# Kernel optimization log

Hardware: AMD Instinct MI355X
Metric: run time of the kernel (lower is better)

The kernel has to match this reference:

```python
import jax, jax.numpy as jnp
import numpy as np

N_NODES = 100000
F_IN = 128
HID = 64
N_EDGES = 1600000
N_PAIRS = 500000


def setup_inputs() -> dict:
    key = jax.random.key(0)
    ks = jax.random.split(key, 12)
    x = jax.random.normal(ks[0], (N_NODES, F_IN), dtype=jnp.float32)
    edge_index = jax.random.randint(ks[1], (2, N_EDGES), 0, N_NODES, dtype=jnp.int32)
    edge_pairs = jax.random.randint(ks[2], (2, N_PAIRS), 0, N_NODES, dtype=jnp.int32)
    # GCNConv weights (glorot-ish scale) and biases
    W1 = jax.random.normal(ks[3], (F_IN, HID), dtype=jnp.float32) / np.sqrt(F_IN)
    b1 = jnp.zeros((HID,), dtype=jnp.float32)
    W2 = jax.random.normal(ks[4], (HID, HID), dtype=jnp.float32) / np.sqrt(HID)
    b2 = jnp.zeros((HID,), dtype=jnp.float32)
    # link predictor MLP: Linear(2H -> H), ReLU, Linear(H -> 1), Sigmoid
    lpW1 = jax.random.normal(ks[5], (2 * HID, HID), dtype=jnp.float32) / np.sqrt(2 * HID)
    lpb1 = jnp.zeros((HID,), dtype=jnp.float32)
    lpW2 = jax.random.normal(ks[6], (HID, 1), dtype=jnp.float32) / np.sqrt(HID)
    lpb2 = jnp.zeros((1,), dtype=jnp.float32)
    return {"x": x, "edge_index": edge_index, "edge_pairs": edge_pairs,
            "W1": W1, "b1": b1, "W2": W2, "b2": b2,
            "lpW1": lpW1, "lpb1": lpb1, "lpW2": lpW2, "lpb2": lpb2}


def _gcn_layer(h, W, b, row, col, deg_inv_sqrt, n_nodes):
    # PyG GCNConv: h' = D^{-1/2} (A + I) D^{-1/2} (h W) + b
    h = h @ W                                   # [N, out]
    norm = deg_inv_sqrt[row] * deg_inv_sqrt[col]  # [E']
    msg = h[row] * norm[:, None]                # gather + scale, [E', out]
    out = jax.ops.segment_sum(msg, col, num_segments=n_nodes)
    return out + b


def reference(x, edge_index, edge_pairs, W1, b1, W2, b2, lpW1, lpb1, lpW2, lpb2):
    n = x.shape[0]
    # add self-loops once (shared by both layers since graph is fixed)
    loop = jnp.arange(n, dtype=edge_index.dtype)
    row = jnp.concatenate([edge_index[0], loop])
    col = jnp.concatenate([edge_index[1], loop])
    deg = jnp.zeros((n,), dtype=x.dtype).at[col].add(1.0)
    deg_inv_sqrt = jnp.where(deg > 0, jax.lax.rsqrt(jnp.maximum(deg, 1.0)), 0.0)

    h = _gcn_layer(x, W1, b1, row, col, deg_inv_sqrt, n)
    h = jax.nn.relu(h)            # dropout is identity at inference
    h = _gcn_layer(h, W2, b2, row, col, deg_inv_sqrt, n)

    # link scorer: gather node pairs, concat, MLP, sigmoid
    z = jnp.concatenate([h[edge_pairs[0]], h[edge_pairs[1]]], axis=1)  # [P, 2H]
    z = jax.nn.relu(z @ lpW1 + lpb1)
    logits = z @ lpW2 + lpb2      # [P, 1]
    return jax.nn.sigmoid(logits).squeeze(-1)
```

## Files before the change

### kernel.cpp

```cpp
#include <hip/hip_runtime.h>
#include <cstddef>
#include <cstdint>

typedef float f4 __attribute__((ext_vector_type(4)));
typedef unsigned short us4 __attribute__((ext_vector_type(4)));
typedef short s8v __attribute__((ext_vector_type(8)));

#define HID 64
#define EPB 4096
#define CAP2 16384

__device__ inline float b2f(unsigned short u) {
    union { unsigned u32; float f; } x; x.u32 = (unsigned)u << 16; return x.f;
}
__device__ inline unsigned short f2b(float f) {
    union { float f; unsigned u; } x; x.f = f;
    unsigned r = 0x7FFFu + ((x.u >> 16) & 1u);
    return (unsigned short)((x.u + r) >> 16);
}
__device__ inline f4 b2f4(us4 h) { f4 r; r[0]=b2f(h[0]); r[1]=b2f(h[1]); r[2]=b2f(h[2]); r[3]=b2f(h[3]); return r; }
__device__ inline us4 f2b4(f4 v) { us4 r; r[0]=f2b(v[0]); r[1]=f2b(v[1]); r[2]=f2b(v[2]); r[3]=f2b(v[3]); return r; }

__device__ inline f4 ld4(const float* p) { return *(const f4*)p; }
__device__ inline f4 ld4(const unsigned short* p) { return b2f4(*(const us4*)p); }
__device__ inline void st4(float* p, f4 v) { *(f4*)p = v; }
__device__ inline void st4(unsigned short* p, f4 v) { *(us4*)p = f2b4(v); }

__global__ __launch_bounds__(256) void k_initcur(int* gcur) {
    int i = blockIdx.x * 256 + threadIdx.x;
    if (i < 512) gcur[i] = i * CAP2;
}

__global__ __launch_bounds__(512) void k_partB(const int* __restrict__ row,
                                               const int* __restrict__ col,
                                               int* __restrict__ gcur,
                                               unsigned* __restrict__ buf, int E) {
    __shared__ int h[512];
    __shared__ int lo[512];
    __shared__ int lb[512];
    __shared__ int lcur[512];
    __shared__ unsigned lbuf[EPB];
    __shared__ unsigned short bk[EPB];
    int t = threadIdx.x;
    h[t] = 0;
    __syncthreads();
    int e0 = blockIdx.x * EPB, e1 = min(E, e0 + EPB);
    for (int i = e0 + t * 4; i < e1; i += 2048) {
        int4 c = *(const int4*)(col + i);
        atomicAdd(&h[c.x >> 9], 1);
        atomicAdd(&h[c.y >> 9], 1);
        atomicAdd(&h[c.z >> 9], 1);
        atomicAdd(&h[c.w >> 9], 1);
    }
    __syncthreads();
    int v = h[t];
    lo[t] = v;
    __syncthreads();
    for (int o = 1; o < 512; o <<= 1) {
        int x = (t >= o) ? lo[t - o] : 0;
        __syncthreads();
        lo[t] += x;
        __syncthreads();
    }
    int excl = lo[t] - v;
    lb[t] = v ? atomicAdd(&gcur[t], v) : 0;
    __syncthreads();
    lo[t] = excl;
    lcur[t] = excl;
    __syncthreads();
    for (int i = e0 + t * 4; i < e1; i += 2048) {
        int4 c = *(const int4*)(col + i);
        int4 r = *(const int4*)(row + i);
        int b0 = c.x >> 9; int p0 = atomicAdd(&lcur[b0], 1);
        lbuf[p0] = ((unsigned)(c.x & 511) << 17) | (unsigned)r.x; bk[p0] = (unsigned short)b0;
        int b1 = c.y >> 9; int p1 = atomicAdd(&lcur[b1], 1);
        lbuf[p1] = ((unsigned)(c.y & 511) << 17) | (unsigned)r.y; bk[p1] = (unsigned short)b1;
        int b2 = c.z >> 9; int p2 = atomicAdd(&lcur[b2], 1);
        lbuf[p2] = ((unsigned)(c.z & 511) << 17) | (unsigned)r.z; bk[p2] = (unsigned short)b2;
        int b3 = c.w >> 9; int p3 = atomicAdd(&lcur[b3], 1);
        lbuf[p3] = ((unsigned)(c.w & 511) << 17) | (unsigned)r.w; bk[p3] = (unsigned short)b3;
    }
    __syncthreads();
    int n = e1 - e0;
    for (int i = t; i < n; i += 512) {
        int b = bk[i];
        buf[lb[b] + (i - lo[b])] = lbuf[i];
    }
}

__global__ __launch_bounds__(512) void k_scanB(const int* __restrict__ gcur,
                                               int* __restrict__ gbase, int NB, int E) {
    __shared__ int s[512];
    int t = threadIdx.x;
    int v = (t < NB) ? (gcur[t] - t * CAP2) : 0;
    s[t] = v;
    __syncthreads();
    for (int o = 1; o < 512; o <<= 1) {
        int x = (t >= o) ? s[t - o] : 0;
        __syncthreads();
        s[t] += x;
        __syncthreads();
    }
    if (t < NB) gbase[t] = s[t] - v;
    if (t == 0) gbase[NB] = E;
}

__global__ __launch_bounds__(512) void k_passC(const unsigned* __restrict__ buf,
                                               const int* __restrict__ gcur,
                                               const int* __restrict__ gbase,
                                               int* __restrict__ rowptr,
                                               int* __restrict__ srcs,
                                               float* __restrict__ dis, int N, int E) {
    __shared__ unsigned sbuf[CAP2];
    __shared__ int hist[512];
    __shared__ int off[512];
    __shared__ int cur[512];
    int b = blockIdx.x, t = threadIdx.x;
    int r0 = b * CAP2, r1 = gcur[b];
    int n = r1 - r0;
    int w0 = gbase[b];
    hist[t] = 0;
    __syncthreads();
    for (int i = r0 + t; i < r1; i += 512) atomicAdd(&hist[(buf[i] >> 17) & 511], 1);
    __syncthreads();
    int v = hist[t];
    off[t] = v;
    __syncthreads();
    for (int o = 1; o < 512; o <<= 1) {
        int x = (t >= o) ? off[t - o] : 0;
        __syncthreads();
        off[t] += x;
        __syncthreads();
    }
    int excl = off[t] - v;
    int gc = b * 512 + t;
    if (gc < N) {
        rowptr[gc] = w0 + excl;
        dis[gc] = rsqrtf(1.0f + (float)v);
    }
    if (b == (int)gridDim.x - 1 && t == 0) rowptr[N] = E;
    cur[t] = excl;
    __syncthreads();
    for (int i = r0 + t; i < r1; i += 512) {
        unsigned u = buf[i];
        int pos = atomicAdd(&cur[(u >> 17) & 511], 1);
        sbuf[pos] = u & 0x1FFFF;
    }
    __syncthreads();
    for (int i = t; i < n; i += 512) srcs[w0 + i] = (int)sbuf[i];
}

template<int K, int NC, typename TIN>
__global__ __launch_bounds__(256) void k_gemmM(
    const TIN* __restrict__ X, const float* __restrict__ W,
    const float* __restrict__ bias, const float* __restrict__ scale,
    unsigned short* __restrict__ outA, unsigned short* __restrict__ outB, int N)
{
    constexpr int KP = K + 8;
    __shared__ unsigned short xs[64][KP];
    __shared__ unsigned short wt[NC][KP];
    const int t = threadIdx.x;
    const int lane = t & 63;
    const int wv = t >> 6;
    const int nbase = blockIdx.x * 64;

    if constexpr (sizeof(TIN) == 4) {
        for (int idx = t; idx < 64 * K / 4; idx += 256) {
            int row = idx / (K / 4);
            int kc = (idx % (K / 4)) * 4;
            int g = nbase + row;
            f4 v = {0.f, 0.f, 0.f, 0.f};
            if (g < N) v = *(const f4*)((const float*)X + (size_t)g * K + kc);
            *(us4*)&xs[row][kc] = f2b4(v);
        }
    } else {
        for (int idx = t; idx < 64 * K / 8; idx += 256) {
            int row = idx / (K / 8);
            int kc = (idx % (K / 8)) * 8;
            int g = nbase + row;
            uint4 v = {0u, 0u, 0u, 0u};
            if (g < N) v = *(const uint4*)((const unsigned short*)X + (size_t)g * K + kc);
            *(uint4*)&xs[row][kc] = v;
        }
    }
    constexpr int WROWS = K * NC / 64;
    for (int idx = t; idx < WROWS * 16; idx += 256) {
        int ks = idx >> 4;
        int c4 = (idx & 15) * 4;
        f4 v = *(const f4*)(W + (size_t)ks * 64 + c4);
        int cofs = (NC == 128 && ks >= K) ? 64 : 0;
        int kk = ks & (K - 1);
        #pragma unroll
        for (int j = 0; j < 4; ++j)
            wt[c4 + j + cofs][kk] = f2b(v[j]);
    }
    __syncthreads();

    constexpr int NT = NC / 16;
    f4 acc[NT];
    #pragma unroll
    for (int i = 0; i < NT; ++i) acc[i] = (f4){0.f, 0.f, 0.f, 0.f};

    const int l15 = lane & 15;
    const int kbase = (lane >> 4) * 8;
    #pragma unroll
    for (int kt = 0; kt < K / 32; ++kt) {
        s8v a = *(const s8v*)&xs[wv * 16 + l15][kt * 32 + kbase];
        #pragma unroll
        for (int ct = 0; ct < NT; ++ct) {
            s8v b = *(const s8v*)&wt[ct * 16 + l15][kt * 32 + kbase];
            acc[ct] = __builtin_amdgcn_mfma_f32_16x16x32_bf16(a, b, acc[ct], 0, 0, 0);
        }
    }

    const int r0 = (lane >> 4) * 4;
    #pragma unroll
    for (int r = 0; r < 4; ++r) {
        int g = nbase + wv * 16 + r0 + r;
        if (g >= N) continue;
        float sc = scale ? scale[g] : 1.0f;
        #pragma unroll
        for (int ct = 0; ct < NT; ++ct) {
            int c = ct * 16 + l15;
            float v = acc[ct][r] * sc;
            if (c < 64) {
                if (bias) v += bias[c];
                outA[(size_t)g * 64 + c] = f2b(v);
            } else {
                outB[(size_t)g * 64 + (c - 64)] = f2b(v);
            }
        }
    }
}

__global__ __launch_bounds__(256) void k_gather(
    const unsigned short* __restrict__ g, const int* __restrict__ rowptr,
    const int* __restrict__ srcs, const float* __restrict__ dis,
    const float* __restrict__ bias, unsigned short* __restrict__ out, int N, int do_relu)
{
    int t = blockIdx.x * 256 + threadIdx.x;
    int node = t >> 4;
    if (node >= N) return;
    int c4 = (t & 15) * 4;

    f4 a0 = ld4(g + (size_t)node * HID + c4);
    f4 a1 = {0.f, 0.f, 0.f, 0.f};
    f4 a2 = {0.f, 0.f, 0.f, 0.f};
    f4 a3 = {0.f, 0.f, 0.f, 0.f};
    int s = rowptr[node], e = rowptr[node + 1];
    for (; s + 3 < e; s += 4) {
        int r0 = srcs[s], r1 = srcs[s + 1], r2 = srcs[s + 2], r3 = srcs[s + 3];
        a0 += ld4(g + (size_t)r0 * HID + c4);
        a1 += ld4(g + (size_t)r1 * HID + c4);
        a2 += ld4(g + (size_t)r2 * HID + c4);
        a3 += ld4(g + (size_t)r3 * HID + c4);
    }
    for (; s < e; ++s) a0 += ld4(g + (size_t)srcs[s] * HID + c4);
    a0 = (a0 + a1) + (a2 + a3);

    float sc = dis[node];
    f4 r;
    #pragma unroll
    for (int j = 0; j < 4; ++j) {
        r[j] = a0[j] * sc + bias[c4 + j];
        if (do_relu) r[j] = r[j] > 0.f ? r[j] : 0.f;
    }
    st4(out + (size_t)node * HID + c4, r);
}

template<int K, typename TIN, typename TOUT>
__global__ __launch_bounds__(256) void k_gemm(
    const TIN* __restrict__ X, const float* __restrict__ W,
    const float* __restrict__ bias, const float* __restrict__ scale,
    TOUT* __restrict__ out1, TOUT* __restrict__ out2, int N)
{
    __shared__ float xs[64][68];
    __shared__ float ws[64][64];
    const int t = threadIdx.x;
    const int nbase = blockIdx.x * 64;
    const int c4 = (t & 15) * 4;
    const int n4 = (t >> 4) * 4;

    float acc[4][4] = {{0.f,0.f,0.f,0.f},{0.f,0.f,0.f,0.f},{0.f,0.f,0.f,0.f},{0.f,0.f,0.f,0.f}};

    const int node = t & 63;
    const int gn = nbase + node;
    const TIN* Xrow = (gn < N) ? (X + (size_t)gn * K) : nullptr;
    const f4* W4 = (const f4*)W;

    for (int kt = 0; kt < K / 64; ++kt) {
        __syncthreads();
        #pragma unroll
        for (int i = 0; i < 4; ++i) {
            int k4r = i * 4 + (t >> 6);
            f4 v = {0.f, 0.f, 0.f, 0.f};
            if (Xrow) v = ld4(Xrow + (size_t)(kt * 16 + k4r) * 4);
            xs[k4r * 4 + 0][node] = v[0];
            xs[k4r * 4 + 1][node] = v[1];
            xs[k4r * 4 + 2][node] = v[2];
            xs[k4r * 4 + 3][node] = v[3];
        }
        #pragma unroll
        for (int i = 0; i < 4; ++i) {
            int f = i * 256 + t;
            int k = f >> 4, m4 = f & 15;
            *(f4*)&ws[k][m4 * 4] = W4[(size_t)(kt * 64 + k) * 16 + m4];
        }
        __syncthreads();
        #pragma unroll 8
        for (int k = 0; k < 64; ++k) {
            f4 xv = *(const f4*)&xs[k][n4];
            f4 wv = *(const f4*)&ws[k][c4];
            #pragma unroll
            for (int i2 = 0; i2 < 4; ++i2)
                #pragma unroll
                for (int j = 0; j < 4; ++j)
                    acc[i2][j] += xv[i2] * wv[j];
        }
    }

    #pragma unroll
    for (int i = 0; i < 4; ++i) {
        int g = nbase + n4 + i;
        if (g < N) {
            float s = scale ? scale[g] : 1.0f;
            f4 r;
            #pragma unroll
            for (int j = 0; j < 4; ++j) {
                float b = bias ? bias[c4 + j] : 0.0f;
                r[j] = acc[i][j] * s + b;
            }
            st4(out1 + (size_t)g * HID + c4, r);
            if (out2) st4(out2 + (size_t)g * HID + c4, r);
        }
    }
}

template<typename TIN>
__global__ __launch_bounds__(256) void k_gemm2(
    const TIN* __restrict__ X, const float* __restrict__ W,
    const float* __restrict__ bias,
    unsigned short* __restrict__ outA, unsigned short* __restrict__ outB, int N)
{
    __shared__ float xs[64][68];
    __shared__ float ws[64][128];
    const int t = threadIdx.x;
    const int nbase = blockIdx.x * 64;
    const int c4 = (t & 15) * 4;
    const int n4 = (t >> 4) * 4;

    float accA[4][4] = {{0.f,0.f,0.f,0.f},{0.f,0.f,0.f,0.f},{0.f,0.f,0.f,0.f},{0.f,0.f,0.f,0.f}};
    float accB[4][4] = {{0.f,0.f,0.f,0.f},{0.f,0.f,0.f,0.f},{0.f,0.f,0.f,0.f},{0.f,0.f,0.f,0.f}};

    const int node = t & 63;
    const int gn = nbase + node;
    const TIN* Xrow = (gn < N) ? (X + (size_t)gn * HID) : nullptr;
    const f4* W4 = (const f4*)W;

    #pragma unroll
    for (int i = 0; i < 4; ++i) {
        int k4r = i * 4 + (t >> 6);
        f4 v = {0.f, 0.f, 0.f, 0.f};
        if (Xrow) v = ld4(Xrow + (size_t)k4r * 4);
        xs[k4r * 4 + 0][node] = v[0];
        xs[k4r * 4 + 1][node] = v[1];
        xs[k4r * 4 + 2][node] = v[2];
        xs[k4r * 4 + 3][node] = v[3];
    }
    #pragma unroll
    for (int i = 0; i < 8; ++i) {
        int f = i * 256 + t;
        int r = f >> 4, m4 = f & 15;
        int k = r & 63, half = (r >> 6) * 64;
        *(f4*)&ws[k][half + m4 * 4] = W4[f];
    }
    __syncthreads();
    #pragma unroll 8
    for (int k = 0; k < 64; ++k) {
        f4 xv = *(const f4*)&xs[k][n4];
        f4 wa = *(const f4*)&ws[k][c4];
        f4 wb = *(const f4*)&ws[k][64 + c4];
        #pragma unroll
        for (int i2 = 0; i2 < 4; ++i2)
            #pragma unroll
            for (int j = 0; j < 4; ++j) {
                accA[i2][j] += xv[i2] * wa[j];
                accB[i2][j] += xv[i2] * wb[j];
            }
    }

    #pragma unroll
    for (int i = 0; i < 4; ++i) {
        int g = nbase + n4 + i;
        if (g < N) {
            f4 ra, rb;
            #pragma unroll
            for (int j = 0; j < 4; ++j) {
                ra[j] = accA[i][j] + bias[c4 + j];
                rb[j] = accB[i][j];
            }
            st4(outA + (size_t)g * HID + c4, ra);
            st4(outB + (size_t)g * HID + c4, rb);
        }
    }
}

__global__ __launch_bounds__(256) void k_count(const int* __restrict__ col,
                                               float* __restrict__ deg, int E) {
    int e = blockIdx.x * 256 + threadIdx.x;
    if (e < E) unsafeAtomicAdd(&deg[col[e]], 1.0f);
}
__global__ __launch_bounds__(256) void k_initf(float* p, float v, int n) {
    int i = blockIdx.x * 256 + threadIdx.x;
    if (i < n) p[i] = v;
}
__global__ __launch_bounds__(256) void k_rsqrt(float* deg, int N) {
    int i = blockIdx.x * 256 + threadIdx.x;
    if (i < N) deg[i] = rsqrtf(deg[i]);
}
__global__ __launch_bounds__(256) void k_scatter(
    const float* __restrict__ g, const int* __restrict__ row, const int* __restrict__ col,
    float* __restrict__ acc, int E)
{
    int t = blockIdx.x * 256 + threadIdx.x;
    int e = t >> 4;
    if (e >= E) return;
    int c4 = (t & 15) * 4;
    int r = row[e], c = col[e];
    f4 v = *(const f4*)(g + (size_t)r * HID + c4);
    float* dst = acc + (size_t)c * HID + c4;
    unsafeAtomicAdd(dst + 0, v[0]);
    unsafeAtomicAdd(dst + 1, v[1]);
    unsafeAtomicAdd(dst + 2, v[2]);
    unsafeAtomicAdd(dst + 3, v[3]);
}
__global__ __launch_bounds__(256) void k_finish(
    const float* __restrict__ acc, const float* __restrict__ dis, const float* __restrict__ bias,
    float* __restrict__ out, int N, int do_relu)
{
    int t = blockIdx.x * 256 + threadIdx.x;
    if (t >= N * 16) return;
    int node = t >> 4, c4 = (t & 15) * 4;
    float s = dis[node];
    f4 v = *(const f4*)(acc + (size_t)t * 4);
    f4 r;
    #pragma unroll
    for (int j = 0; j < 4; ++j) {
        r[j] = v[j] * s + bias[c4 + j];
        if (do_relu) r[j] = r[j] > 0.f ? r[j] : 0.f;
    }
    *(f4*)(out + (size_t)t * 4) = r;
}

__global__ __launch_bounds__(256) void k_pair(
    const unsigned short* __restrict__ A, const unsigned short* __restrict__ B,
    const int* __restrict__ pairs, const float* __restrict__ w2, const float* __restrict__ b2,
    float* __restrict__ out, int P)
{
    __shared__ float w2s[64];
    if (threadIdx.x < 64) w2s[threadIdx.x] = w2[threadIdx.x];
    __syncthreads();
    int gidx = blockIdx.x * 256 + threadIdx.x;
    int grp = gidx >> 4;
    int p0 = grp * 2, p1 = p0 + 1;
    if (p0 >= P) return;
    int l = gidx & 15;
    int sub = l & 7;
    int isB = l >> 3;
    const unsigned short* base = isB ? B : A;
    const int* pp = isB ? (pairs + P) : pairs;

    int n0 = pp[p0];
    int4 o0 = *(const int4*)(base + (size_t)n0 * HID + sub * 8);
    bool has1 = (p1 < P);
    int4 o1 = {0, 0, 0, 0};
    if (has1) {
        int n1 = pp[p1];
        o1 = *(const int4*)(base + (size_t)n1 * HID + sub * 8);
    }

    int4 q0, q1;
    q0.x = __shfl_xor(o0.x, 8, 16); q0.y = __shfl_xor(o0.y, 8, 16);
    q0.z = __shfl_xor(o0.z, 8, 16); q0.w = __shfl_xor(o0.w, 8, 16);
    q1.x = __shfl_xor(o1.x, 8, 16); q1.y = __shfl_xor(o1.y, 8, 16);
    q1.z = __shfl_xor(o1.z, 8, 16); q1.w = __shfl_xor(o1.w, 8, 16);

    const float* wv = &w2s[sub * 8];
    int oa0[4] = {o0.x, o0.y, o0.z, o0.w};
    int ob0[4] = {q0.x, q0.y, q0.z, q0.w};
    int oa1[4] = {o1.x, o1.y, o1.z, o1.w};
    int ob1[4] = {q1.x, q1.y, q1.z, q1.w};
    float acc0 = 0.f, acc1 = 0.f;
    #pragma unroll
    for (int k = 0; k < 4; ++k) {
        float alo = __uint_as_float((unsigned)oa0[k] << 16);
        float ahi = __uint_as_float((unsigned)oa0[k] & 0xFFFF0000u);
        float blo = __uint_as_float((unsigned)ob0[k] << 16);
        float bhi = __uint_as_float((unsigned)ob0[k] & 0xFFFF0000u);
        float zlo = alo + blo; zlo = zlo > 0.f ? zlo : 0.f;
        float zhi = ahi + bhi; zhi = zhi > 0.f ? zhi : 0.f;
        acc0 += zlo * wv[2 * k] + zhi * wv[2 * k + 1];

        float clo = __uint_as_float((unsigned)oa1[k] << 16);
        float chi = __uint_as_float((unsigned)oa1[k] & 0xFFFF0000u);
        float dlo = __uint_as_float((unsigned)ob1[k] << 16);
        float dhi = __uint_as_float((unsigned)ob1[k] & 0xFFFF0000u);
        float ylo = clo + dlo; ylo = ylo > 0.f ? ylo : 0.f;
        float yhi = chi + dhi; yhi = yhi > 0.f ? yhi : 0.f;
        acc1 += ylo * wv[2 * k] + yhi * wv[2 * k + 1];
    }
    acc0 += __shfl_xor(acc0, 1, 16);
    acc0 += __shfl_xor(acc0, 2, 16);
    acc0 += __shfl_xor(acc0, 4, 16);
    acc1 += __shfl_xor(acc1, 1, 16);
    acc1 += __shfl_xor(acc1, 2, 16);
    acc1 += __shfl_xor(acc1, 4, 16);
    if (l == 0) {
        float bb = b2[0];
        out[p0] = 1.0f / (1.0f + __expf(-(acc0 + bb)));
        if (has1) out[p1] = 1.0f / (1.0f + __expf(-(acc1 + bb)));
    }
}

extern "C" void kernel_launch(void* const* d_in, const int* in_sizes, int n_in,
                              void* d_out, int out_size, void* d_ws, size_t ws_size,
                              hipStream_t stream)
{
    if (n_in < 11) return;
    const float* x    = (const float*)d_in[0];
    const int*   ei   = (const int*)d_in[1];
    const int*   ep   = (const int*)d_in[2];
    const float* W1   = (const float*)d_in[3];
    const float* b1   = (const float*)d_in[4];
    const float* W2   = (const float*)d_in[5];
    const float* b2   = (const float*)d_in[6];
    const float* lpW1 = (const float*)d_in[7];
    const float* lpb1 = (const float*)d_in[8];
    const float* lpW2 = (const float*)d_in[9];
    const float* lpb2 = (const float*)d_in[10];
    const int N = in_sizes[0] / 128;
    const int E = in_sizes[1] / 2;
    const int P = in_sizes[2] / 2;
    const int* erow = ei;
    const int* ecol = ei + E;
    float* out = (float*)d_out;

    const int gb  = (N + 63) / 64;
    const int hb  = (N * 16 + 255) / 256;
    const int NB2 = (N + 511) / 512;
    const int pa  = (E + EPB - 1) / EPB;
    const int pb  = (int)(((size_t)((P + 1) / 2) * 16 + 255) / 256);

    char* w = (char*)d_ws;
    float* dis    = (float*)w;  w += (size_t)N * 4;
    int*   rowptr = (int*)w;    w += ((size_t)N + 1) * 4;
    int*   gbase  = (int*)w;    w += 513 * 4;
    int*   gcur   = (int*)w;    w += 512 * 4;
    int*   srcs   = (int*)w;    w += (size_t)E * 4;
    size_t off = ((size_t)(w - (char*)d_ws) + 255) & ~(size_t)255;

    size_t featB = (size_t)N * HID * 2;
    unsigned short* bufA = (unsigned short*)((char*)d_ws + off);
    unsigned short* bufB = bufA + (size_t)N * HID;
    size_t need = off + 2 * featB;

    bool useNew = (N <= 131072) && (NB2 <= 512) && (ws_size >= need) &&
                  ((size_t)E <= 20 * (size_t)N) && (E % 4 == 0) &&
                  ((size_t)NB2 * CAP2 * 4 <= 2 * featB);

    if (useNew) {
        unsigned* pbuf = (unsigned*)bufA;

        k_initcur<<<2, 256, 0, stream>>>(gcur);
        k_partB<<<pa, 512, 0, stream>>>(erow, ecol, gcur, pbuf, E);
        k_scanB<<<1, 512, 0, stream>>>(gcur, gbase, NB2, E);
        k_passC<<<NB2, 512, 0, stream>>>(pbuf, gcur, gbase, rowptr, srcs, dis, N, E);

        k_gemmM<128, 64, float><<<gb, 256, 0, stream>>>(x, W1, nullptr, dis, bufA, nullptr, N);
        k_gather<<<hb, 256, 0, stream>>>(bufA, rowptr, srcs, dis, b1, bufB, N, 1);
        k_gemmM<64, 64, unsigned short><<<gb, 256, 0, stream>>>(bufB, W2, nullptr, dis, bufA, nullptr, N);
        k_gather<<<hb, 256, 0, stream>>>(bufA, rowptr, srcs, dis, b2, bufB, N, 0);
        k_gemmM<64, 128, unsigned short><<<gb, 256, 0, stream>>>(bufB, lpW1, lpb1, nullptr, bufA, bufB, N);

        k_pair<<<pb, 256, 0, stream>>>(bufA, bufB, ep, lpW2, lpb2, out, P);
    } else {
        size_t off_fb = (((size_t)N + 512) * 4 + 255) & ~(size_t)255;
        float* fA = (float*)((char*)d_ws + off_fb);
        float* fB = fA + (size_t)N * HID;
        if (ws_size < off_fb + 2 * (size_t)N * HID * 4) return;
        const int nb = (N + 255) / 256;
        const int eb = (E + 255) / 256;
        const int sb = (int)(((size_t)E * 16 + 255) / 256);
        k_initf<<<nb, 256, 0, stream>>>(dis, 1.0f, N);
        k_count<<<eb, 256, 0, stream>>>(ecol, dis, E);
        k_rsqrt<<<nb, 256, 0, stream>>>(dis, N);
        k_gemm<128, float, float><<<gb, 256, 0, stream>>>(x, W1, nullptr, dis, fA, fB, N);
        k_scatter<<<sb, 256, 0, stream>>>(fA, erow, ecol, fB, E);
        k_finish<<<hb, 256, 0, stream>>>(fB, dis, b1, fB, N, 1);
        k_gemm<64, float, float><<<gb, 256, 0, stream>>>(fB, W2, nullptr, dis, fA, fB, N);
        k_scatter<<<sb, 256, 0, stream>>>(fA, erow, ecol, fB, E);
        k_finish<<<hb, 256, 0, stream>>>(fB, dis, b2, fB, N, 0);
        unsigned short* bA = (unsigned short*)fA;
        unsigned short* bB = bA + (size_t)N * HID;
        k_gemm2<float><<<gb, 256, 0, stream>>>(fB, lpW1, lpb1, bA, bB, N);
        k_pair<<<pb, 256, 0, stream>>>(bA, bB, ep, lpW2, lpb2, out, P);
    }
}
```

Measured before the change: 194.1 us.

## Fuse edge partition with first GEMM and fold bucket scan into passC

New measurement: 175.4 us. 9.6% less time.

```diff
diff --git a/kernel.cpp b/kernel.cpp
--- a/kernel.cpp
+++ b/kernel.cpp
@@ -9,6 +9,7 @@
 #define HID 64
 #define EPB 4096
 #define CAP2 16384
+#define SMEM_BYTES 52224
 
 __device__ inline float b2f(unsigned short u) {
     union { unsigned u32; float f; } x; x.u32 = (unsigned)u << 16; return x.f;
@@ -31,94 +32,147 @@
     if (i < 512) gcur[i] = i * CAP2;
 }
 
-__global__ __launch_bounds__(512) void k_partB(const int* __restrict__ row,
-                                               const int* __restrict__ col,
-                                               int* __restrict__ gcur,
-                                               unsigned* __restrict__ buf, int E) {
-    __shared__ int h[512];
-    __shared__ int lo[512];
-    __shared__ int lb[512];
-    __shared__ int lcur[512];
-    __shared__ unsigned lbuf[EPB];
-    __shared__ unsigned short bk[EPB];
-    int t = threadIdx.x;
-    h[t] = 0;
-    __syncthreads();
-    int e0 = blockIdx.x * EPB, e1 = min(E, e0 + EPB);
-    for (int i = e0 + t * 4; i < e1; i += 2048) {
-        int4 c = *(const int4*)(col + i);
-        atomicAdd(&h[c.x >> 9], 1);
-        atomicAdd(&h[c.y >> 9], 1);
-        atomicAdd(&h[c.z >> 9], 1);
-        atomicAdd(&h[c.w >> 9], 1);
-    }
-    __syncthreads();
-    int v = h[t];
-    lo[t] = v;
-    __syncthreads();
-    for (int o = 1; o < 512; o <<= 1) {
-        int x = (t >= o) ? lo[t - o] : 0;
-        __syncthreads();
-        lo[t] += x;
-        __syncthreads();
-    }
-    int excl = lo[t] - v;
-    lb[t] = v ? atomicAdd(&gcur[t], v) : 0;
-    __syncthreads();
-    lo[t] = excl;
-    lcur[t] = excl;
-    __syncthreads();
-    for (int i = e0 + t * 4; i < e1; i += 2048) {
-        int4 c = *(const int4*)(col + i);
-        int4 r = *(const int4*)(row + i);
-        int b0 = c.x >> 9; int p0 = atomicAdd(&lcur[b0], 1);
-        lbuf[p0] = ((unsigned)(c.x & 511) << 17) | (unsigned)r.x; bk[p0] = (unsigned short)b0;
-        int b1 = c.y >> 9; int p1 = atomicAdd(&lcur[b1], 1);
-        lbuf[p1] = ((unsigned)(c.y & 511) << 17) | (unsigned)r.y; bk[p1] = (unsigned short)b1;
-        int b2 = c.z >> 9; int p2 = atomicAdd(&lcur[b2], 1);
-        lbuf[p2] = ((unsigned)(c.z & 511) << 17) | (unsigned)r.z; bk[p2] = (unsigned short)b2;
-        int b3 = c.w >> 9; int p3 = atomicAdd(&lcur[b3], 1);
-        lbuf[p3] = ((unsigned)(c.w & 511) << 17) | (unsigned)r.w; bk[p3] = (unsigned short)b3;
-    }
-    __syncthreads();
-    int n = e1 - e0;
-    for (int i = t; i < n; i += 512) {
-        int b = bk[i];
-        buf[lb[b] + (i - lo[b])] = lbuf[i];
-    }
-}
-
-__global__ __launch_bounds__(512) void k_scanB(const int* __restrict__ gcur,
-                                               int* __restrict__ gbase, int NB, int E) {
-    __shared__ int s[512];
-    int t = threadIdx.x;
-    int v = (t < NB) ? (gcur[t] - t * CAP2) : 0;
-    s[t] = v;
-    __syncthreads();
-    for (int o = 1; o < 512; o <<= 1) {
-        int x = (t >= o) ? s[t - o] : 0;
-        __syncthreads();
-        s[t] += x;
-        __syncthreads();
-    }
-    if (t < NB) gbase[t] = s[t] - v;
-    if (t == 0) gbase[NB] = E;
+__global__ __launch_bounds__(512) void k_fused1(
+    const int* __restrict__ row, const int* __restrict__ col,
+    int* __restrict__ gcur, unsigned* __restrict__ buf, int E,
+    const float* __restrict__ X, const float* __restrict__ W,
+    unsigned short* __restrict__ outA, int N, int PA)
+{
+    __shared__ __align__(16) char smem[SMEM_BYTES];
+    const int t = threadIdx.x;
+
+    if ((int)blockIdx.x < PA) {
+        int* h    = (int*)smem;
+        int* lo   = h + 512;
+        int* lb   = lo + 512;
+        int* lcur = lb + 512;
+        unsigned* lbuf = (unsigned*)(smem + 8192);
+        unsigned short* bk = (unsigned short*)(smem + 24576);
+
+        h[t] = 0;
+        __syncthreads();
+        int e0 = blockIdx.x * EPB, e1 = min(E, e0 + EPB);
+        for (int i = e0 + t * 4; i < e1; i += 2048) {
+            int4 c = *(const int4*)(col + i);
+            atomicAdd(&h[c.x >> 9], 1);
+            atomicAdd(&h[c.y >> 9], 1);
+            atomicAdd(&h[c.z >> 9], 1);
+            atomicAdd(&h[c.w >> 9], 1);
+        }
+        __syncthreads();
+        int v = h[t];
+        lo[t] = v;
+        __syncthreads();
+        for (int o = 1; o < 512; o <<= 1) {
+            int x2 = (t >= o) ? lo[t - o] : 0;
+            __syncthreads();
+            lo[t] += x2;
+            __syncthreads();
+        }
+        int excl = lo[t] - v;
+        lb[t] = v ? atomicAdd(&gcur[t], v) : 0;
+        __syncthreads();
+        lo[t] = excl;
+        lcur[t] = excl;
+        __syncthreads();
+        for (int i = e0 + t * 4; i < e1; i += 2048) {
+            int4 c = *(const int4*)(col + i);
+            int4 r = *(const int4*)(row + i);
+            int b0 = c.x >> 9; int p0 = atomicAdd(&lcur[b0], 1);
+            lbuf[p0] = ((unsigned)(c.x & 511) << 17) | (unsigned)r.x; bk[p0] = (unsigned short)b0;
+            int b1 = c.y >> 9; int p1 = atomicAdd(&lcur[b1], 1);
+            lbuf[p1] = ((unsigned)(c.y & 511) << 17) | (unsigned)r.y; bk[p1] = (unsigned short)b1;
+            int b2 = c.z >> 9; int p2 = atomicAdd(&lcur[b2], 1);
+            lbuf[p2] = ((unsigned)(c.z & 511) << 17) | (unsigned)r.z; bk[p2] = (unsigned short)b2;
+            int b3 = c.w >> 9; int p3 = atomicAdd(&lcur[b3], 1);
+            lbuf[p3] = ((unsigned)(c.w & 511) << 17) | (unsigned)r.w; bk[p3] = (unsigned short)b3;
+        }
+        __syncthreads();
+        int n = e1 - e0;
+        for (int i = t; i < n; i += 512) {
+            int b = bk[i];
+            buf[lb[b] + (i - lo[b])] = lbuf[i];
+        }
+    } else {
+        constexpr int KP = 136;
+        unsigned short* xs = (unsigned short*)smem;
+        unsigned short* wt = (unsigned short*)(smem + 34816);
+        const int nbase = ((int)blockIdx.x - PA) * 128;
+
+        for (int idx = t; idx < 4096; idx += 512) {
+            int r = idx >> 5;
+            int kc = (idx & 31) * 4;
+            int g = nbase + r;
+            f4 v = {0.f, 0.f, 0.f, 0.f};
+            if (g < N) v = *(const f4*)(X + (size_t)g * 128 + kc);
+            *(us4*)&xs[r * KP + kc] = f2b4(v);
+        }
+        for (int idx = t; idx < 2048; idx += 512) {
+            int ks = idx >> 4;
+            int c4 = (idx & 15) * 4;
+            f4 v = *(const f4*)(W + (size_t)ks * 64 + c4);
+            #pragma unroll
+            for (int j = 0; j < 4; ++j)
+                wt[(c4 + j) * KP + ks] = f2b(v[j]);
+        }
+        __syncthreads();
+
+        const int lane = t & 63;
+        const int wv = t >> 6;
+        const int l15 = lane & 15;
+        const int kb = (lane >> 4) * 8;
+        f4 acc[4];
+        #pragma unroll
+        for (int i = 0; i < 4; ++i) acc[i] = (f4){0.f, 0.f, 0.f, 0.f};
+        #pragma unroll
+        for (int kt = 0; kt < 4; ++kt) {
+            s8v a = *(const s8v*)&xs[(wv * 16 + l15) * KP + kt * 32 + kb];
+            #pragma unroll
+            for (int ct = 0; ct < 4; ++ct) {
+                s8v b = *(const s8v*)&wt[(ct * 16 + l15) * KP + kt * 32 + kb];
+                acc[ct] = __builtin_amdgcn_mfma_f32_16x16x32_bf16(a, b, acc[ct], 0, 0, 0);
+            }
+        }
+        const int r0 = (lane >> 4) * 4;
+        #pragma unroll
+        for (int r = 0; r < 4; ++r) {
+            int g = nbase + wv * 16 + r0 + r;
+            if (g >= N) continue;
+            #pragma unroll
+            for (int ct = 0; ct < 4; ++ct) {
+                int c = ct * 16 + l15;
+                outA[(size_t)g * 64 + c] = f2b(acc[ct][r]);
+            }
+        }
+    }
 }
 
 __global__ __launch_bounds__(512) void k_passC(const unsigned* __restrict__ buf,
                                                const int* __restrict__ gcur,
-                                               const int* __restrict__ gbase,
                                                int* __restrict__ rowptr,
                                                int* __restrict__ srcs,
-                                               float* __restrict__ dis, int N, int E) {
+                                               float* __restrict__ dis, int N, int E, int NB) {
     __shared__ unsigned sbuf[CAP2];
     __shared__ int hist[512];
     __shared__ int off[512];
     __shared__ int cur[512];
     int b = blockIdx.x, t = threadIdx.x;
+
+    int c0 = (t < NB) ? (gcur[t] - t * CAP2) : 0;
+    off[t] = c0;
+    __syncthreads();
+    for (int o = 1; o < 512; o <<= 1) {
+        int x = (t >= o) ? off[t - o] : 0;
+        __syncthreads();
+        off[t] += x;
+        __syncthreads();
+    }
+    int w0 = (b == 0) ? 0 : off[b - 1];
+    if (b == 0 && t == 0) rowptr[N] = E;
+    __syncthreads();
+
     int r0 = b * CAP2, r1 = gcur[b];
     int n = r1 - r0;
-    int w0 = gbase[b];
     hist[t] = 0;
     __syncthreads();
     for (int i = r0 + t; i < r1; i += 512) atomicAdd(&hist[(buf[i] >> 17) & 511], 1);
@@ -138,7 +192,6 @@
         rowptr[gc] = w0 + excl;
         dis[gc] = rsqrtf(1.0f + (float)v);
     }
-    if (b == (int)gridDim.x - 1 && t == 0) rowptr[N] = E;
     cur[t] = excl;
     __syncthreads();
     for (int i = r0 + t; i < r1; i += 512) {
@@ -236,29 +289,40 @@
 __global__ __launch_bounds__(256) void k_gather(
     const unsigned short* __restrict__ g, const int* __restrict__ rowptr,
     const int* __restrict__ srcs, const float* __restrict__ dis,
-    const float* __restrict__ bias, unsigned short* __restrict__ out, int N, int do_relu)
+    const float* __restrict__ bias, unsigned short* __restrict__ out,
+    int N, int do_relu, int scale_src)
 {
     int t = blockIdx.x * 256 + threadIdx.x;
     int node = t >> 4;
     if (node >= N) return;
     int c4 = (t & 15) * 4;
 
-    f4 a0 = ld4(g + (size_t)node * HID + c4);
-    f4 a1 = {0.f, 0.f, 0.f, 0.f};
-    f4 a2 = {0.f, 0.f, 0.f, 0.f};
-    f4 a3 = {0.f, 0.f, 0.f, 0.f};
+    float sc = dis[node];
+    f4 a0, a1 = {0.f,0.f,0.f,0.f}, a2 = {0.f,0.f,0.f,0.f}, a3 = {0.f,0.f,0.f,0.f};
     int s = rowptr[node], e = rowptr[node + 1];
-    for (; s + 3 < e; s += 4) {
-        int r0 = srcs[s], r1 = srcs[s + 1], r2 = srcs[s + 2], r3 = srcs[s + 3];
-        a0 += ld4(g + (size_t)r0 * HID + c4);
-        a1 += ld4(g + (size_t)r1 * HID + c4);
-        a2 += ld4(g + (size_t)r2 * HID + c4);
-        a3 += ld4(g + (size_t)r3 * HID + c4);
-    }
-    for (; s < e; ++s) a0 += ld4(g + (size_t)srcs[s] * HID + c4);
+    if (scale_src) {
+        a0 = ld4(g + (size_t)node * HID + c4) * sc;
+        for (; s + 3 < e; s += 4) {
+            int r0 = srcs[s], r1 = srcs[s + 1], r2 = srcs[s + 2], r3 = srcs[s + 3];
+            a0 += ld4(g + (size_t)r0 * HID + c4) * dis[r0];
+            a1 += ld4(g + (size_t)r1 * HID + c4) * dis[r1];
+            a2 += ld4(g + (size_t)r2 * HID + c4) * dis[r2];
+            a3 += ld4(g + (size_t)r3 * HID + c4) * dis[r3];
+        }
+        for (; s < e; ++s) { int r0 = srcs[s]; a0 += ld4(g + (size_t)r0 * HID + c4) * dis[r0]; }
+    } else {
+        a0 = ld4(g + (size_t)node * HID + c4);
+        for (; s + 3 < e; s += 4) {
+            int r0 = srcs[s], r1 = srcs[s + 1], r2 = srcs[s + 2], r3 = srcs[s + 3];
+            a0 += ld4(g + (size_t)r0 * HID + c4);
+            a1 += ld4(g + (size_t)r1 * HID + c4);
+            a2 += ld4(g + (size_t)r2 * HID + c4);
+            a3 += ld4(g + (size_t)r3 * HID + c4);
+        }
+        for (; s < e; ++s) a0 += ld4(g + (size_t)srcs[s] * HID + c4);
+    }
     a0 = (a0 + a1) + (a2 + a3);
 
-    float sc = dis[node];
     f4 r;
     #pragma unroll
     for (int j = 0; j < 4; ++j) {
@@ -546,6 +610,7 @@
     float* out = (float*)d_out;
 
     const int gb  = (N + 63) / 64;
+    const int gb2 = (N + 127) / 128;
     const int hb  = (N * 16 + 255) / 256;
     const int NB2 = (N + 511) / 512;
     const int pa  = (E + EPB - 1) / EPB;
@@ -554,10 +619,11 @@
     char* w = (char*)d_ws;
     float* dis    = (float*)w;  w += (size_t)N * 4;
     int*   rowptr = (int*)w;    w += ((size_t)N + 1) * 4;
-    int*   gbase  = (int*)w;    w += 513 * 4;
     int*   gcur   = (int*)w;    w += 512 * 4;
     int*   srcs   = (int*)w;    w += (size_t)E * 4;
-    size_t off = ((size_t)(w - (char*)d_ws) + 255) & ~(size_t)255;
+    size_t offb = ((size_t)(w - (char*)d_ws) + 255) & ~(size_t)255;
+    unsigned* buf = (unsigned*)((char*)d_ws + offb);
+    size_t off = (offb + (size_t)NB2 * CAP2 * 4 + 255) & ~(size_t)255;
 
     size_t featB = (size_t)N * HID * 2;
     unsigned short* bufA = (unsigned short*)((char*)d_ws + off);
@@ -565,21 +631,16 @@
     size_t need = off + 2 * featB;
 
     bool useNew = (N <= 131072) && (NB2 <= 512) && (ws_size >= need) &&
-                  ((size_t)E <= 20 * (size_t)N) && (E % 4 == 0) &&
-                  ((size_t)NB2 * CAP2 * 4 <= 2 * featB);
+                  ((size_t)E <= 20 * (size_t)N) && (E % 4 == 0);
 
     if (useNew) {
-        unsigned* pbuf = (unsigned*)bufA;
-
         k_initcur<<<2, 256, 0, stream>>>(gcur);
-        k_partB<<<pa, 512, 0, stream>>>(erow, ecol, gcur, pbuf, E);
-        k_scanB<<<1, 512, 0, stream>>>(gcur, gbase, NB2, E);
-        k_passC<<<NB2, 512, 0, stream>>>(pbuf, gcur, gbase, rowptr, srcs, dis, N, E);
-
-        k_gemmM<128, 64, float><<<gb, 256, 0, stream>>>(x, W1, nullptr, dis, bufA, nullptr, N);
-        k_gather<<<hb, 256, 0, stream>>>(bufA, rowptr, srcs, dis, b1, bufB, N, 1);
+        k_fused1<<<pa + gb2, 512, 0, stream>>>(erow, ecol, gcur, buf, E, x, W1, bufA, N, pa);
+        k_passC<<<NB2, 512, 0, stream>>>(buf, gcur, rowptr, srcs, dis, N, E, NB2);
+
+        k_gather<<<hb, 256, 0, stream>>>(bufA, rowptr, srcs, dis, b1, bufB, N, 1, 1);
         k_gemmM<64, 64, unsigned short><<<gb, 256, 0, stream>>>(bufB, W2, nullptr, dis, bufA, nullptr, N);
-        k_gather<<<hb, 256, 0, stream>>>(bufA, rowptr, srcs, dis, b2, bufB, N, 0);
+        k_gather<<<hb, 256, 0, stream>>>(bufA, rowptr, srcs, dis, b2, bufB, N, 0, 0);
         k_gemmM<64, 128, unsigned short><<<gb, 256, 0, stream>>>(bufB, lpW1, lpb1, nullptr, bufA, bufB, N);
 
         k_pair<<<pb, 256, 0, stream>>>(bufA, bufB, ep, lpW2, lpb2, out, P);
```
